# Optimization experiments

Measured on AMD Instinct MI355X. Metric: run time of the kernel, lower is better.

## Reference

```python
import jax, jax.numpy as jnp
import numpy as np

B, N, D = 8, 4096, 3

def setup_inputs() -> dict:
    key = jax.random.key(0)
    k1, k2 = jax.random.split(key)
    prediction = jax.random.normal(k1, (B, N, D), dtype=jnp.float32)
    ground_truth = jax.random.normal(k2, (B, N, D), dtype=jnp.float32)
    return {"prediction": prediction, "ground_truth": ground_truth}

def reference(prediction, ground_truth):
    batch_size, num, _ = prediction.shape
    # T[b, i, j] = ||pred[b, i] - gt[b, j]||^2  -> [B, N, N]
    diff = prediction[:, :, None, :] - ground_truth[:, None, :, :]
    T = jnp.sum(diff * diff, axis=-1)
    # squeeze() in torch is a no-op for B > 1
    cd_loss = jnp.sum(jnp.min(T, axis=1)) + jnp.sum(jnp.min(T, axis=2))
    return cd_loss / batch_size
```

## Files before the change

### kernel.cpp

```cpp
#include <hip/hip_runtime.h>

#define TPB 256
#define IPT 8
#define NIB 2
#define NPTS 4096
#define NB 8

__global__ __launch_bounds__(TPB, 4) void cd_partial_kernel(
    const float* __restrict__ pred, const float* __restrict__ gt,
    float* __restrict__ partial, int njb, int jchunk) {
  extern __shared__ float4 sg[];

  int bid = blockIdx.x;
  int jb  = bid % njb;  bid /= njb;
  int ib  = bid & (NIB - 1); bid /= NIB;
  int b   = bid & (NB - 1);  bid /= NB;
  int dir = bid;

  const float* src = (dir == 0) ? pred : gt;
  const float* tgt = (dir == 0) ? gt : pred;
  src += (size_t)b * NPTS * 3;
  tgt += (size_t)b * NPTS * 3;

  const int t = threadIdx.x;

  for (int p = t; p < jchunk; p += TPB) {
    int j = jb * jchunk + p;
    float gx = tgt[j * 3 + 0];
    float gy = tgt[j * 3 + 1];
    float gz = tgt[j * 3 + 2];
    sg[p] = make_float4(gx, gy, gz, fmaf(gx, gx, fmaf(gy, gy, gz * gz)));
  }

  float qx[IPT], qy[IPT], qz[IPT], pp[IPT], mn[IPT];
  const int ibase = ib * (TPB * IPT);
#pragma unroll
  for (int k = 0; k < IPT; ++k) {
    int i = ibase + k * TPB + t;
    float x = src[i * 3 + 0];
    float y = src[i * 3 + 1];
    float z = src[i * 3 + 2];
    qx[k] = -2.0f * x;
    qy[k] = -2.0f * y;
    qz[k] = -2.0f * z;
    pp[k] = fmaf(x, x, fmaf(y, y, z * z));
    mn[k] = 3.4e38f;
  }
  __syncthreads();

#pragma unroll 4
  for (int p = 0; p < jchunk; p += 2) {
    float4 g0 = sg[p];
    float4 g1 = sg[p + 1];
#pragma unroll
    for (int k = 0; k < IPT; ++k) {
      float v0 = fmaf(qx[k], g0.x, fmaf(qy[k], g0.y, fmaf(qz[k], g0.z, g0.w)));
      float v1 = fmaf(qx[k], g1.x, fmaf(qy[k], g1.y, fmaf(qz[k], g1.z, g1.w)));
      mn[k] = fminf(mn[k], fminf(v0, v1));
    }
  }

  float* outp = partial + ((size_t)((dir * NB + b) * njb + jb)) * NPTS;
#pragma unroll
  for (int k = 0; k < IPT; ++k) {
    outp[ibase + k * TPB + t] = mn[k] + pp[k];
  }
}

__global__ __launch_bounds__(TPB) void cd_reduce_kernel(
    const float* __restrict__ partial, float* __restrict__ out, int njb) {
  const int total = 2 * NB * NPTS;
  int tid = blockIdx.x * TPB + threadIdx.x;
  float local = 0.0f;
  for (int s = tid; s < total; s += gridDim.x * TPB) {
    int db = s >> 12;
    int i  = s & (NPTS - 1);
    const float* p = partial + (size_t)db * njb * NPTS + i;
    float m = p[0];
    for (int jb = 1; jb < njb; ++jb) m = fminf(m, p[(size_t)jb * NPTS]);
    local += m;
  }
#pragma unroll
  for (int off = 32; off > 0; off >>= 1) local += __shfl_down(local, off, 64);
  __shared__ float red[TPB / 64];
  int wave = threadIdx.x >> 6;
  int lane = threadIdx.x & 63;
  if (lane == 0) red[wave] = local;
  __syncthreads();
  if (threadIdx.x == 0) {
    float s = 0.0f;
    for (int w = 0; w < TPB / 64; ++w) s += red[w];
    atomicAdd(out, s * (1.0f / NB));
  }
}

extern "C" void kernel_launch(void* const* d_in, const int* in_sizes, int n_in,
                              void* d_out, int out_size, void* d_ws, size_t ws_size,
                              hipStream_t stream) {
  const float* pred = (const float*)d_in[0];
  const float* gt   = (const float*)d_in[1];
  float* out        = (float*)d_out;
  float* partial    = (float*)d_ws;

  int njb = 32;
  {
    size_t per_jb = (size_t)2 * NB * NPTS * sizeof(float);
    size_t need = per_jb * njb;
    if (ws_size < need) {
      njb = (int)(ws_size / per_jb);
      if (njb < 1) njb = 1;
      while (njb & (njb - 1)) njb &= njb - 1;
      if (njb > 32) njb = 32;
    }
  }
  int jchunk = NPTS / njb;

  hipMemsetAsync(d_out, 0, sizeof(float), stream);

  dim3 grid(2 * NB * NIB * njb);
  size_t lds = (size_t)jchunk * sizeof(float4);
  cd_partial_kernel<<<grid, TPB, lds, stream>>>(pred, gt, partial, njb, jchunk);
  cd_reduce_kernel<<<256, TPB, 0, stream>>>(partial, out, njb);
}
```

Measured before the change: 43.02 us.

## Fold output zeroing into kernel, vectorize point IO, double j-splitting

```diff
diff --git a/kernel.cpp b/kernel.cpp
--- a/kernel.cpp
+++ b/kernel.cpp
@@ -6,10 +6,12 @@
 #define NPTS 4096
 #define NB 8
 
-__global__ __launch_bounds__(TPB, 4) void cd_partial_kernel(
+__global__ __launch_bounds__(TPB, 6) void cd_partial_kernel(
     const float* __restrict__ pred, const float* __restrict__ gt,
-    float* __restrict__ partial, int njb, int jchunk) {
+    float* __restrict__ partial, float* __restrict__ out, int njb, int jchunk) {
   extern __shared__ float4 sg[];
+
+  if (blockIdx.x == 0 && threadIdx.x == 0) *out = 0.0f;
 
   int bid = blockIdx.x;
   int jb  = bid % njb;  bid /= njb;
@@ -32,18 +34,26 @@
     sg[p] = make_float4(gx, gy, gz, fmaf(gx, gx, fmaf(gy, gy, gz * gz)));
   }
 
+  const int ibase = ib * (TPB * IPT);
+  const float4* sv = (const float4*)(src + (size_t)(ibase + t * IPT) * 3);
+  float4 A = sv[0], B2 = sv[1], C = sv[2], D = sv[3], E = sv[4], F = sv[5];
+  float x[IPT], y[IPT], z[IPT];
+  x[0]=A.x;  y[0]=A.y;  z[0]=A.z;
+  x[1]=A.w;  y[1]=B2.x; z[1]=B2.y;
+  x[2]=B2.z; y[2]=B2.w; z[2]=C.x;
+  x[3]=C.y;  y[3]=C.z;  z[3]=C.w;
+  x[4]=D.x;  y[4]=D.y;  z[4]=D.z;
+  x[5]=D.w;  y[5]=E.x;  z[5]=E.y;
+  x[6]=E.z;  y[6]=E.w;  z[6]=F.x;
+  x[7]=F.y;  y[7]=F.z;  z[7]=F.w;
+
   float qx[IPT], qy[IPT], qz[IPT], pp[IPT], mn[IPT];
-  const int ibase = ib * (TPB * IPT);
 #pragma unroll
   for (int k = 0; k < IPT; ++k) {
-    int i = ibase + k * TPB + t;
-    float x = src[i * 3 + 0];
-    float y = src[i * 3 + 1];
-    float z = src[i * 3 + 2];
-    qx[k] = -2.0f * x;
-    qy[k] = -2.0f * y;
-    qz[k] = -2.0f * z;
-    pp[k] = fmaf(x, x, fmaf(y, y, z * z));
+    qx[k] = -2.0f * x[k];
+    qy[k] = -2.0f * y[k];
+    qz[k] = -2.0f * z[k];
+    pp[k] = fmaf(x[k], x[k], fmaf(y[k], y[k], z[k] * z[k]));
     mn[k] = 3.4e38f;
   }
   __syncthreads();
@@ -60,11 +70,11 @@
     }
   }
 
-  float* outp = partial + ((size_t)((dir * NB + b) * njb + jb)) * NPTS;
-#pragma unroll
-  for (int k = 0; k < IPT; ++k) {
-    outp[ibase + k * TPB + t] = mn[k] + pp[k];
-  }
+  float* outp = partial + ((size_t)((dir * NB + b) * njb + jb)) * NPTS + ibase + t * IPT;
+  float4 s0 = make_float4(mn[0] + pp[0], mn[1] + pp[1], mn[2] + pp[2], mn[3] + pp[3]);
+  float4 s1 = make_float4(mn[4] + pp[4], mn[5] + pp[5], mn[6] + pp[6], mn[7] + pp[7]);
+  ((float4*)outp)[0] = s0;
+  ((float4*)outp)[1] = s1;
 }
 
 __global__ __launch_bounds__(TPB) void cd_reduce_kernel(
@@ -77,6 +87,7 @@
     int i  = s & (NPTS - 1);
     const float* p = partial + (size_t)db * njb * NPTS + i;
     float m = p[0];
+#pragma unroll 8
     for (int jb = 1; jb < njb; ++jb) m = fminf(m, p[(size_t)jb * NPTS]);
     local += m;
   }
@@ -102,7 +113,7 @@
   float* out        = (float*)d_out;
   float* partial    = (float*)d_ws;
 
-  int njb = 32;
+  int njb = 64;
   {
     size_t per_jb = (size_t)2 * NB * NPTS * sizeof(float);
     size_t need = per_jb * njb;
@@ -110,15 +121,13 @@
       njb = (int)(ws_size / per_jb);
       if (njb < 1) njb = 1;
       while (njb & (njb - 1)) njb &= njb - 1;
-      if (njb > 32) njb = 32;
+      if (njb > 64) njb = 64;
     }
   }
   int jchunk = NPTS / njb;
 
-  hipMemsetAsync(d_out, 0, sizeof(float), stream);
-
   dim3 grid(2 * NB * NIB * njb);
   size_t lds = (size_t)jchunk * sizeof(float4);
-  cd_partial_kernel<<<grid, TPB, lds, stream>>>(pred, gt, partial, njb, jchunk);
+  cd_partial_kernel<<<grid, TPB, lds, stream>>>(pred, gt, partial, out, njb, jchunk);
   cd_reduce_kernel<<<256, TPB, 0, stream>>>(partial, out, njb);
 }
```

After: 45.95 us. 1.07x slower.
